# Optimization experiments

Hardware: AMD Instinct MI355X
Metric: run time of the kernel (lower is better)

## Reference

```python
import jax, jax.numpy as jnp
import numpy as np

V, E, H, Ld, NL = 32000, 256, 512, 512, 2   # vocab, embed, enc hidden, latent (=dec hidden), layers
S, T = 1024, 512                            # encoder src len, decoder target len


def setup_inputs() -> dict:
    key = jax.random.key(0)
    ks = jax.random.split(key, 20)
    n = lambda k, shp: jax.random.normal(k, shp, dtype=jnp.float32) * 0.05
    return {
        "x": jax.random.randint(ks[0], (S,), 0, V),
        "y": jax.random.randint(ks[1], (T,), 0, V),
        "emb": n(ks[2], (V, E)),
        # encoder LSTM (input E -> hidden H, 2 layers); bias = b_ih + b_hh combined
        "enc_Wih0": n(ks[3], (4 * H, E)), "enc_Whh0": n(ks[4], (4 * H, H)), "enc_b0": n(ks[5], (4 * H,)),
        "enc_Wih1": n(ks[6], (4 * H, H)), "enc_Whh1": n(ks[7], (4 * H, H)), "enc_b1": n(ks[8], (4 * H,)),
        "enc_fcW": n(ks[9], (Ld, H)), "enc_fcb": n(ks[10], (Ld,)),
        # decoder LSTM: input size is 1 (token id as float!), hidden Ld, 2 layers
        "dec_Wih0": n(ks[11], (4 * Ld, 1)), "dec_Whh0": n(ks[12], (4 * Ld, Ld)), "dec_b0": n(ks[13], (4 * Ld,)),
        "dec_Wih1": n(ks[14], (4 * Ld, Ld)), "dec_Whh1": n(ks[15], (4 * Ld, Ld)), "dec_b1": n(ks[16], (4 * Ld,)),
        "dec_fcW": n(ks[17], (V, Ld)), "dec_fcb": n(ks[18], (V,)),
    }


def _cell(x_in, h, c, Wih, Whh, b):
    # torch LSTM gate order: i, f, g, o
    g = Wih @ x_in + Whh @ h + b
    i, f, gg, o = jnp.split(g, 4)
    c2 = jax.nn.sigmoid(f) * c + jax.nn.sigmoid(i) * jnp.tanh(gg)
    h2 = jax.nn.sigmoid(o) * jnp.tanh(c2)
    return h2, c2


def reference(x, y, emb,
              enc_Wih0, enc_Whh0, enc_b0, enc_Wih1, enc_Whh1, enc_b1,
              enc_fcW, enc_fcb,
              dec_Wih0, dec_Whh0, dec_b0, dec_Wih1, dec_Whh1, dec_b1,
              dec_fcW, dec_fcb):
    encW = [(enc_Wih0, enc_Whh0, enc_b0), (enc_Wih1, enc_Whh1, enc_b1)]
    decW = [(dec_Wih0, dec_Whh0, dec_b0), (dec_Wih1, dec_Whh1, dec_b1)]

    # ---- Encoder: embed + 2-layer LSTM over the source, keep final h ----
    em = emb[x]  # [S, E]

    def enc_step(carry, e_t):
        h, c = carry  # each [NL, H]
        inp = e_t
        hs, cs = [], []
        for l in range(NL):
            Wih, Whh, b = encW[l]
            hl, cl = _cell(inp, h[l], c[l], Wih, Whh, b)
            hs.append(hl); cs.append(cl)
            inp = hl
        return (jnp.stack(hs), jnp.stack(cs)), None

    init = (jnp.zeros((NL, H), jnp.float32), jnp.zeros((NL, H), jnp.float32))
    (h_enc, _), _ = jax.lax.scan(enc_step, init, em)

    z = jax.nn.relu(enc_fcW @ h_enc[-1] + enc_fcb)        # [Ld]
    h0 = jnp.tile(z[None, :], (NL, 1))                    # torch.cat([fc]*num_layers)
    c0 = h0                                               # h_c_enc = h_s_initial in source

    def dec_step(carry, _):
        tok, h, c = carry  # tok: scalar float token id, h/c: [NL, Ld]
        inp = tok[None]    # x.reshape(-1,1).to(float32) with one token -> input dim 1
        hs, cs = [], []
        for l in range(NL):
            Wih, Whh, b = decW[l]
            hl, cl = _cell(inp, h[l], c[l], Wih, Whh, b)
            hs.append(hl); cs.append(cl)
            inp = hl
        logits = dec_fcW @ hs[-1] + dec_fcb               # [V]
        nxt = jnp.argmax(logits).astype(jnp.float32)      # best_guess
        return (nxt, jnp.stack(hs), jnp.stack(cs)), logits

    tok0 = y[0].astype(jnp.float32)
    _, logits_seq = jax.lax.scan(dec_step, (tok0, h0, c0), None, length=T - 1)  # [T-1, V]

    # outputs[0] stays zeros, as in the source (loop starts at i=1); training mode -> raw logits
    return jnp.concatenate([jnp.zeros((1, V), jnp.float32), logits_seq], axis=0)
```

## Files before the change

kernel.cpp:

```cpp
#include <hip/hip_runtime.h>
#include <cmath>

#define NWG 256
#define NTHR 1024

static constexpr int kV = 32000;
static constexpr int kS = 1024;
static constexpr int kT = 512;

static constexpr int kLdsRows = 61;

static constexpr int kOffH0  = kLdsRows * 512;
static constexpr int kOffH1  = kOffH0 + 512;
static constexpr int kOffG   = kOffH1 + 512;
static constexpr int kOffPK  = kOffG + 16;
static constexpr int kOffTok = kOffPK + 32;
static constexpr int kOffB   = kOffTok + 1;
static constexpr int kSmemFloats = kOffB + kLdsRows;
static constexpr unsigned kSmemBytes = ((kSmemFloats * 4 + 255) / 256) * 256;

struct SeqParams {
  const int* x; const int* y;
  const float* emb;
  const float* eWih0; const float* eWhh0; const float* eb0;
  const float* eWih1; const float* eWhh1; const float* eb1;
  const float* efcW;  const float* efcb;
  const float* dWih0; const float* dWhh0; const float* db0;
  const float* dWih1; const float* dWhh1; const float* db1;
  const float* dfcW;  const float* dfcb;
  float* out;
  float* P0;
  unsigned long long* h0e;
  unsigned long long* h1e;
  unsigned long long* h0dB;
  unsigned long long* h1dB;
  unsigned long long* candB;
  unsigned* arrive;
  unsigned* go;
  int decApp;
};

__device__ __forceinline__ float sigmf(float v) { return 1.0f / (1.0f + expf(-v)); }

__device__ __forceinline__ float g_ld(const float* p_) {
  return __hip_atomic_load(p_, __ATOMIC_RELAXED, __HIP_MEMORY_SCOPE_AGENT);
}
__device__ __forceinline__ void g_st(float* p_, float v) {
  __hip_atomic_store(p_, v, __ATOMIC_RELAXED, __HIP_MEMORY_SCOPE_AGENT);
}
__device__ __forceinline__ unsigned long long g_ld64(const unsigned long long* p_) {
  return __hip_atomic_load(p_, __ATOMIC_RELAXED, __HIP_MEMORY_SCOPE_AGENT);
}
__device__ __forceinline__ void g_st64(unsigned long long* p_, unsigned long long v) {
  __hip_atomic_store(p_, v, __ATOMIC_RELAXED, __HIP_MEMORY_SCOPE_AGENT);
}

__device__ __forceinline__ float dot4(float4 a, float4 b) {
  return a.x * b.x + a.y * b.y + a.z * b.z + a.w * b.w;
}
__device__ __forceinline__ float wred(float a) {
  a += __shfl_down(a, 32);
  a += __shfl_down(a, 16);
  a += __shfl_down(a, 8);
  a += __shfl_down(a, 4);
  a += __shfl_down(a, 2);
  a += __shfl_down(a, 1);
  return a;
}
__device__ __forceinline__ int swzg(int g) { return g ^ ((g >> 3) & 7); }

__device__ __forceinline__ void pub_write(unsigned long long* pub, int idx,
                                          unsigned tag, float v) {
  g_st64(&pub[idx],
         ((unsigned long long)tag << 32) | (unsigned long long)__float_as_uint(v));
}

template <int SLP>
__device__ __forceinline__ void poll_stage(const unsigned long long* pub,
                                           unsigned tag, float* dst,
                                           int wave8, int lane) {
  const int idx = (wave8 << 6) | lane;
  unsigned long long x;
  for (;;) {
    x = g_ld64(&pub[idx]);
    if (__all((unsigned)(x >> 32) == tag)) break;
    __builtin_amdgcn_s_sleep(SLP);
  }
  dst[idx] = __uint_as_float((unsigned)x);
}

__device__ __forceinline__ unsigned long long* hrow(unsigned long long* b,
                                                    int app, int s) {
  return b + (size_t)(app ? s : (s & 1)) * 512;
}
__device__ __forceinline__ unsigned long long* crow(unsigned long long* b,
                                                    int app, int t) {
  return b + (app ? (size_t)t * 256 : 0);
}

__device__ void grid_barrier(const SeqParams& p, unsigned gen) {
  __syncthreads();
  const int tid = threadIdx.x;
  if (blockIdx.x == 0) {
    if (tid > 0 && tid < 256) {
      while (__hip_atomic_load(&p.arrive[tid * 32], __ATOMIC_RELAXED,
                               __HIP_MEMORY_SCOPE_AGENT) < gen)
        __builtin_amdgcn_s_sleep(1);
    }
    __syncthreads();
    if (tid > 0 && tid < 256) {
      __hip_atomic_store(&p.go[tid * 32], gen, __ATOMIC_RELAXED,
                         __HIP_MEMORY_SCOPE_AGENT);
    }
  } else {
    if (tid == 0) {
      __hip_atomic_store(&p.arrive[blockIdx.x * 32], gen, __ATOMIC_RELAXED,
                         __HIP_MEMORY_SCOPE_AGENT);
      while (__hip_atomic_load(&p.go[blockIdx.x * 32], __ATOMIC_RELAXED,
                               __HIP_MEMORY_SCOPE_AGENT) < gen)
        __builtin_amdgcn_s_sleep(1);
    }
    __syncthreads();
  }
}

__device__ __forceinline__ unsigned long long pack_cand(float a, int row,
                                                        unsigned tag) {
  const unsigned u = __float_as_uint(a);
  const unsigned key = u ^ (unsigned)(((int)u >> 31) | 0x80000000);
  return ((unsigned long long)key << 32) |
         ((unsigned long long)(0x7FFFu ^ (unsigned)row) << 17) |
         (unsigned long long)tag;
}

__global__ __launch_bounds__(NTHR, 4) void seq2seq_kernel(SeqParams p) {
  extern __shared__ float smem[];
  float* lds_w  = smem;
  float* lds_h0 = smem + kOffH0;
  float* lds_h1 = smem + kOffH1;
  float* lds_g  = smem + kOffG;
  unsigned long long* lds_pk =
      reinterpret_cast<unsigned long long*>(smem + kOffPK);
  float* lds_tok = smem + kOffTok;
  float* lds_b   = smem + kOffB;

  const int w = blockIdx.x;
  const int tid = threadIdx.x;
  const int wave = tid >> 6, lane = tid & 63;
  const int app = p.decApp;

  {
    float* lds_em = lds_w;
    const int t0  = (w & 127) * 8;
    const int row = (w >> 7) * 1024 + tid;
    float4* emv = reinterpret_cast<float4*>(lds_em);
    if (tid < 512) {
      const int tl = tid >> 6, kq = tid & 63;
      const int tk = p.x[t0 + tl];
      emv[tid] = reinterpret_cast<const float4*>(p.emb)[(size_t)tk * 64 + kq];
    }
    __syncthreads();
    float acc[8];
    const float b = p.eb0[row];
#pragma unroll
    for (int t = 0; t < 8; ++t) acc[t] = b;
    for (int kc = 0; kc < 4; ++kc) {
      float4 wv[16];
      const float4* wr =
          reinterpret_cast<const float4*>(p.eWih0 + (size_t)row * 256) + kc * 16;
#pragma unroll
      for (int i = 0; i < 16; ++i) wv[i] = wr[i];
#pragma unroll
      for (int t = 0; t < 8; ++t) {
        const float4* ev =
            reinterpret_cast<const float4*>(lds_em + t * 256) + kc * 16;
        float a = acc[t];
#pragma unroll
        for (int i = 0; i < 16; ++i) a += dot4(wv[i], ev[i]);
        acc[t] = a;
      }
    }
#pragma unroll
    for (int t = 0; t < 8; ++t)
      g_st(&p.P0[(size_t)(t0 + t) * 2048 + row], acc[t]);
    if (tid < 4) {
      if (w < 128) pub_write(p.h0e, w * 4 + tid, 1u, 0.f);
      else         pub_write(p.h1e, (w - 128) * 4 + tid, 1u, 0.f);
    }
    __syncthreads();

    const float4* gw4 =
        reinterpret_cast<const float4*>(p.dfcW + (size_t)w * 125 * 512);
    float4* lw4 = reinterpret_cast<float4*>(lds_w);
    for (int i = tid; i < kLdsRows * 128; i += NTHR)
      lw4[(i & ~127) | ((i & 127) ^ ((i >> 3) & 7))] = gw4[i];
    if (tid < kLdsRows) lds_b[tid] = p.dfcb[w * 125 + tid];
  }
  grid_barrier(p, 1u);

  if (w < 128) {
    const int row_l0 = (wave & 3) * 512 + w * 4 + (wave >> 2);
    float pv_next = 0.f;
    if (lane == 0) pv_next = g_ld(&p.P0[row_l0]);
    float c0e = 0.f;
    for (int i = 0; i < kS; ++i) {
      if (wave < 8)
        poll_stage<2>(p.h0e + (size_t)i * 512, (unsigned)(i + 1), lds_h0,
                      wave, lane);
      __syncthreads();
      const float pv = pv_next;
      if (lane == 0 && i + 1 < kS)
        pv_next = g_ld(&p.P0[(size_t)(i + 1) * 2048 + row_l0]);
      const float4* W4 =
          reinterpret_cast<const float4*>(p.eWhh0 + (size_t)row_l0 * 512);
      const float4* h4 = reinterpret_cast<const float4*>(lds_h0);
      float a = dot4(W4[lane * 2], h4[lane * 2]) +
                dot4(W4[lane * 2 + 1], h4[lane * 2 + 1]);
      a = wred(a);
      if (lane == 0) lds_g[wave] = a + pv;
      __syncthreads();
      if (tid < 4) {
        const float gi = lds_g[tid * 4 + 0];
        const float gf = lds_g[tid * 4 + 1];
        const float gg = lds_g[tid * 4 + 2];
        const float go = lds_g[tid * 4 + 3];
        const float c2 = sigmf(gf) * c0e + sigmf(gi) * tanhf(gg);
        c0e = c2;
        pub_write(p.h0e, (int)((size_t)(i + 1) * 512) + w * 4 + tid,
                  (unsigned)(i + 2), sigmf(go) * tanhf(c2));
      }
    }
  } else {
    const int ww = w - 128;
    const int row = (wave & 3) * 512 + ww * 4 + (wave >> 2);
    float c1e = 0.f;
    for (int j = 0; j < kS; ++j) {
      if (wave < 8)
        poll_stage<2>(p.h0e + (size_t)(j + 1) * 512, (unsigned)(j + 2),
                      lds_h0, wave, lane);
      else
        poll_stage<2>(p.h1e + (size_t)j * 512, (unsigned)(j + 1), lds_h1,
                      wave - 8, lane);
      __syncthreads();
      const float4* Wa =
          reinterpret_cast<const float4*>(p.eWih1 + (size_t)row * 512);
      const float4* Wb =
          reinterpret_cast<const float4*>(p.eWhh1 + (size_t)row * 512);
      const float4* h4a = reinterpret_cast<const float4*>(lds_h0);
      const float4* h4b = reinterpret_cast<const float4*>(lds_h1);
      float a = (lane == 0) ? p.eb1[row] : 0.f;
      a += dot4(Wa[lane * 2], h4a[lane * 2]) +
           dot4(Wa[lane * 2 + 1], h4a[lane * 2 + 1]);
      a += dot4(Wb[lane * 2], h4b[lane * 2]) +
           dot4(Wb[lane * 2 + 1], h4b[lane * 2 + 1]);
      a = wred(a);
      if (lane == 0) lds_g[wave] = a;
      __syncthreads();
      if (tid < 4) {
        const float gi = lds_g[tid * 4 + 0];
        const float gf = lds_g[tid * 4 + 1];
        const float gg = lds_g[tid * 4 + 2];
        const float go = lds_g[tid * 4 + 3];
        const float c2 = sigmf(gf) * c1e + sigmf(gi) * tanhf(gg);
        c1e = c2;
        pub_write(p.h1e, (int)((size_t)(j + 1) * 512) + ww * 4 + tid,
                  (unsigned)(j + 2), sigmf(go) * tanhf(c2));
      }
    }
  }

  float c0d = 0.f, c1d = 0.f;
  {
    if (wave < 8)
      poll_stage<2>(p.h1e + (size_t)kS * 512, (unsigned)(kS + 1), lds_h0,
                    wave, lane);
    __syncthreads();
    if (wave < 2) {
      const int u = w * 2 + wave;
      const float4* W4 =
          reinterpret_cast<const float4*>(p.efcW + (size_t)u * 512);
      const float4* h4 = reinterpret_cast<const float4*>(lds_h0);
      float a = dot4(W4[lane * 2], h4[lane * 2]) +
                dot4(W4[lane * 2 + 1], h4[lane * 2 + 1]);
      a = wred(a);
      if (lane == 0) lds_g[wave] = fmaxf(a + p.efcb[u], 0.f);
    }
    __syncthreads();
    if (tid < 2) {
      const int uu = w * 2 + tid;
      const float z = lds_g[tid];
      c0d = z; c1d = z;
      pub_write(hrow(p.h0dB, app, 0), uu, 1u, z);
      pub_write(hrow(p.h1dB, app, 0), uu, 1u, z);
    }
  }

  float4 Ra0, Rb0, Ra1, Rb1, Ra2, Rb2, Ra3, Rb3;
  float bi0, bi1, bi2, bi3;
  {
    const int rb = w * 125 + kLdsRows + wave * 4;
#define LWR(i)                                                                \
  {                                                                           \
    const float4* q =                                                         \
        reinterpret_cast<const float4*>(p.dfcW + (size_t)(rb + i) * 512) +    \
        lane * 2;                                                             \
    Ra##i = q[0];                                                             \
    Rb##i = q[1];                                                             \
    bi##i = p.dfcb[rb + i];                                                   \
  }
    LWR(0) LWR(1) LWR(2) LWR(3)
#undef LWR
  }
  grid_barrier(p, 2u);

  for (int t = 0; t < kT - 1; ++t) {
    {
      if (wave < 8) {
        poll_stage<2>(hrow(p.h0dB, app, t), (unsigned)(t + 1), lds_h0, wave,
                      lane);
      } else if (wave == 15) {
        if (t == 0) {
          if (lane == 0) lds_tok[0] = (float)p.y[0];
        } else {
          const unsigned tagexp = (unsigned)t;
          const unsigned long long* cb = crow(p.candB, app, t);
          unsigned long long k0, k1, k2, k3;
          for (;;) {
            k0 = g_ld64(&cb[lane]);
            k1 = g_ld64(&cb[lane + 64]);
            k2 = g_ld64(&cb[lane + 128]);
            k3 = g_ld64(&cb[lane + 192]);
            const bool ok = ((unsigned)(k0 & 0x1FFFF) == tagexp) &
                            ((unsigned)(k1 & 0x1FFFF) == tagexp) &
                            ((unsigned)(k2 & 0x1FFFF) == tagexp) &
                            ((unsigned)(k3 & 0x1FFFF) == tagexp);
            if (__all(ok)) break;
            __builtin_amdgcn_s_sleep(1);
          }
          unsigned long long pk = k0;
          if (k1 > pk) pk = k1;
          if (k2 > pk) pk = k2;
          if (k3 > pk) pk = k3;
#pragma unroll
          for (int off = 32; off >= 1; off >>= 1) {
            const unsigned long long o = __shfl_down(pk, off);
            if (o > pk) pk = o;
          }
          if (lane == 0)
            lds_tok[0] = (float)(0x7FFFu ^ (unsigned)((pk >> 17) & 0x7FFF));
        }
      }
      __syncthreads();
      if (wave < 8) {
        const int row = (wave & 3) * 512 + w * 2 + (wave >> 2);
        const float4* W4 =
            reinterpret_cast<const float4*>(p.dWhh0 + (size_t)row * 512);
        const float4* h4 = reinterpret_cast<const float4*>(lds_h0);
        float a = dot4(W4[lane * 2], h4[lane * 2]) +
                  dot4(W4[lane * 2 + 1], h4[lane * 2 + 1]);
        a = wred(a);
        if (lane == 0) lds_g[wave] = a;
      }
      __syncthreads();
      if (tid < 2) {
        const float tok = lds_tok[0];
        const int uu = w * 2 + tid;
        float gv[4];
#pragma unroll
        for (int g = 0; g < 4; ++g) {
          const int rg = g * 512 + uu;
          gv[g] = lds_g[tid * 4 + g] + p.dWih0[rg] * tok + p.db0[rg];
        }
        const float c2 = sigmf(gv[1]) * c0d + sigmf(gv[0]) * tanhf(gv[2]);
        c0d = c2;
        pub_write(hrow(p.h0dB, app, t + 1), uu, (unsigned)(t + 2),
                  sigmf(gv[3]) * tanhf(c2));
      }
    }
    {
      if (wave < 8)
        poll_stage<2>(hrow(p.h0dB, app, t + 1), (unsigned)(t + 2), lds_h0,
                      wave, lane);
      else
        poll_stage<2>(hrow(p.h1dB, app, t), (unsigned)(t + 1), lds_h1,
                      wave - 8, lane);
      __syncthreads();
      if (wave < 8) {
        const int row = (wave & 3) * 512 + w * 2 + (wave >> 2);
        const float4* Wa =
            reinterpret_cast<const float4*>(p.dWih1 + (size_t)row * 512);
        const float4* Wb =
            reinterpret_cast<const float4*>(p.dWhh1 + (size_t)row * 512);
        const float4* h4a = reinterpret_cast<const float4*>(lds_h0);
        const float4* h4b = reinterpret_cast<const float4*>(lds_h1);
        float a = (lane == 0) ? p.db1[row] : 0.f;
        a += dot4(Wa[lane * 2], h4a[lane * 2]) +
             dot4(Wa[lane * 2 + 1], h4a[lane * 2 + 1]);
        a += dot4(Wb[lane * 2], h4b[lane * 2]) +
             dot4(Wb[lane * 2 + 1], h4b[lane * 2 + 1]);
        a = wred(a);
        if (lane == 0) lds_g[wave] = a;
      }
      __syncthreads();
      if (tid < 2) {
        const int uu = w * 2 + tid;
        const float gi = lds_g[tid * 4 + 0];
        const float gf = lds_g[tid * 4 + 1];
        const float gg = lds_g[tid * 4 + 2];
        const float go = lds_g[tid * 4 + 3];
        const float c2 = sigmf(gf) * c1d + sigmf(gi) * tanhf(gg);
        c1d = c2;
        pub_write(hrow(p.h1dB, app, t + 1), uu, (unsigned)(t + 2),
                  sigmf(go) * tanhf(c2));
      }
    }
    {
      if (wave < 8)
        poll_stage<2>(hrow(p.h1dB, app, t + 1), (unsigned)(t + 2), lds_h0,
                      wave, lane);
      __syncthreads();
      const float4* h4 = reinterpret_cast<const float4*>(lds_h0);
      const float4 ha = h4[lane * 2], hb = h4[lane * 2 + 1];
      float* orow = p.out + (size_t)(t + 1) * kV;
      const unsigned tagout = (unsigned)(t + 1);
      unsigned long long best = 0;
      const int rb = w * 125 + kLdsRows + wave * 4;
#define FCR(i)                                                                \
  {                                                                           \
    const int row = rb + i;                                                   \
    float a = (lane == 0) ? bi##i : 0.f;                                      \
    a += dot4(Ra##i, ha) + dot4(Rb##i, hb);                                   \
    a = wred(a);                                                              \
    if (lane == 0) {                                                          \
      orow[row] = a;                                                          \
      const unsigned long long pk2 = pack_cand(a, row, tagout);               \
      if (pk2 > best) best = pk2;                                             \
    }                                                                         \
  }
      FCR(0) FCR(1) FCR(2) FCR(3)
#undef FCR
      const float4* lw4 = reinterpret_cast<const float4*>(lds_w);
      for (int rr = wave; rr < kLdsRows; rr += 16) {
        const int row = w * 125 + rr;
        const float4* lwr = lw4 + rr * 128;
        float a = (lane == 0) ? lds_b[rr] : 0.f;
        a += dot4(lwr[swzg(lane * 2)], ha) + dot4(lwr[swzg(lane * 2 + 1)], hb);
        a = wred(a);
        if (lane == 0) {
          orow[row] = a;
          const unsigned long long pk2 = pack_cand(a, row, tagout);
          if (pk2 > best) best = pk2;
        }
      }
      if (lane == 0) lds_pk[wave] = best;
      __syncthreads();
      if (tid == 0) {
        unsigned long long b2 = lds_pk[0];
#pragma unroll
        for (int k2 = 1; k2 < 16; ++k2)
          if (lds_pk[k2] > b2) b2 = lds_pk[k2];
        g_st64(&crow(p.candB, app, (int)tagout)[w], b2);
      }
    }
  }

  {
    const int idx = w * NTHR + tid;
    if (idx < kV) p.out[idx] = 0.f;
  }
}

extern "C" void kernel_launch(void* const* d_in, const int* in_sizes, int n_in,
                              void* d_out, int out_size, void* d_ws, size_t ws_size,
                              hipStream_t stream) {
  (void)in_sizes; (void)n_in; (void)out_size;
  SeqParams P;
  P.x     = (const int*)d_in[0];
  P.y     = (const int*)d_in[1];
  P.emb   = (const float*)d_in[2];
  P.eWih0 = (const float*)d_in[3];
  P.eWhh0 = (const float*)d_in[4];
  P.eb0   = (const float*)d_in[5];
  P.eWih1 = (const float*)d_in[6];
  P.eWhh1 = (const float*)d_in[7];
  P.eb1   = (const float*)d_in[8];
  P.efcW  = (const float*)d_in[9];
  P.efcb  = (const float*)d_in[10];
  P.dWih0 = (const float*)d_in[11];
  P.dWhh0 = (const float*)d_in[12];
  P.db0   = (const float*)d_in[13];
  P.dWih1 = (const float*)d_in[14];
  P.dWhh1 = (const float*)d_in[15];
  P.db1   = (const float*)d_in[16];
  P.dfcW  = (const float*)d_in[17];
  P.dfcb  = (const float*)d_in[18];
  P.out   = (float*)d_out;

  char* ws = (char*)d_ws;
  P.arrive = (unsigned*)ws;
  P.go     = (unsigned*)(ws + 32768);
  unsigned long long* ringC = (unsigned long long*)(ws + 65536);
  unsigned long long* ring0 = (unsigned long long*)(ws + 67584);
  unsigned long long* ring1 = (unsigned long long*)(ws + 75776);

  const size_t dAppO   = 131072ull;
  const size_t kHdB    = 512ull * 512ull * 8ull;
  const size_t kCdB    = 512ull * 256ull * 8ull;
  const size_t dAppEnd = dAppO + 2 * kHdB + kCdB;
  if (ws_size >= dAppEnd) {
    P.h0dB  = (unsigned long long*)(ws + dAppO);
    P.h1dB  = (unsigned long long*)(ws + dAppO + kHdB);
    P.candB = (unsigned long long*)(ws + dAppO + 2 * kHdB);
    P.decApp = 1;
  } else {
    P.h0dB = ring0; P.h1dB = ring1; P.candB = ringC;
    P.decApp = 0;
  }

  const size_t kP0B = 8388608ull;
  const size_t kEpB = 4198400ull;
  const size_t encO = (dAppEnd + 65535ull) & ~65535ull;
  if (ws_size >= encO + kP0B + 2 * kEpB) {
    P.P0  = (float*)(ws + encO);
    P.h0e = (unsigned long long*)(ws + encO + kP0B);
    P.h1e = (unsigned long long*)(ws + encO + kP0B + kEpB);
  } else {
    char* ob = (char*)d_out;
    P.P0  = (float*)ob;
    P.h0e = (unsigned long long*)(ob + kP0B);
    P.h1e = (unsigned long long*)(ob + kP0B + kEpB);
  }

  (void)hipFuncSetAttribute(reinterpret_cast<const void*>(seq2seq_kernel),
                            hipFuncAttributeMaxDynamicSharedMemorySize,
                            (int)kSmemBytes);

  (void)hipMemsetAsync(d_ws, 0, 83968, stream);

  void* args[] = { &P };
  (void)hipLaunchCooperativeKernel(reinterpret_cast<void*>(seq2seq_kernel),
                                   dim3(NWG), dim3(NTHR), args, kSmemBytes,
                                   stream);
}
```

Measured before the change: 5.602 ms.

## Prefetch published hidden states, swizzle LDS h vectors, use lighter workgroup barriers

Polling of the tagged hidden-state publication buffers now starts with a speculative load issued one stage early, so the first check often succeeds without another global round trip. The argmax candidate buffer is also prefetched ahead of time. Hidden vectors written to LDS are now swizzled to avoid bank conflicts on the float4 reads. __syncthreads is replaced by a barrier that only waits on LDS traffic, not global memory. The aim is to cut latency on the serial recurrent critical path, at the cost of extra global traffic and more complex ordering.

New measurement: 6.123 ms. 9.3% more time.

```diff
diff --git a/kernel.cpp b/kernel.cpp
--- a/kernel.cpp
+++ b/kernel.cpp
@@ -68,6 +68,14 @@
   return a;
 }
 __device__ __forceinline__ int swzg(int g) { return g ^ ((g >> 3) & 7); }
+__device__ __forceinline__ int swzf(int idx) {
+  return (swzg(idx >> 2) << 2) | (idx & 3);
+}
+
+__device__ __forceinline__ void wg_sync() {
+  asm volatile("s_waitcnt lgkmcnt(0)" ::: "memory");
+  __builtin_amdgcn_s_barrier();
+}
 
 __device__ __forceinline__ void pub_write(unsigned long long* pub, int idx,
                                           unsigned tag, float v) {
@@ -76,17 +84,14 @@
 }
 
 template <int SLP>
-__device__ __forceinline__ void poll_stage(const unsigned long long* pub,
-                                           unsigned tag, float* dst,
-                                           int wave8, int lane) {
-  const int idx = (wave8 << 6) | lane;
-  unsigned long long x;
-  for (;;) {
+__device__ __forceinline__ unsigned long long resolve64(
+    unsigned long long x, const unsigned long long* pub, unsigned tag,
+    int idx) {
+  while (!__all((unsigned)(x >> 32) == tag)) {
+    __builtin_amdgcn_s_sleep(SLP);
     x = g_ld64(&pub[idx]);
-    if (__all((unsigned)(x >> 32) == tag)) break;
-    __builtin_amdgcn_s_sleep(SLP);
-  }
-  dst[idx] = __uint_as_float((unsigned)x);
+  }
+  return x;
 }
 
 __device__ __forceinline__ unsigned long long* hrow(unsigned long long* b,
@@ -200,25 +205,31 @@
 
   if (w < 128) {
     const int row_l0 = (wave & 3) * 512 + w * 4 + (wave >> 2);
+    const int idx = (wave << 6) | lane;
     float pv_next = 0.f;
     if (lane == 0) pv_next = g_ld(&p.P0[row_l0]);
+    unsigned long long pf = 0;
+    if (wave < 8) pf = g_ld64(&p.h0e[idx]);
     float c0e = 0.f;
     for (int i = 0; i < kS; ++i) {
-      if (wave < 8)
-        poll_stage<2>(p.h0e + (size_t)i * 512, (unsigned)(i + 1), lds_h0,
-                      wave, lane);
-      __syncthreads();
+      if (wave < 8) {
+        const unsigned long long xx =
+            resolve64<2>(pf, p.h0e + (size_t)i * 512, (unsigned)(i + 1), idx);
+        lds_h0[swzf(idx)] = __uint_as_float((unsigned)xx);
+        pf = g_ld64(&p.h0e[(size_t)(i + 1) * 512 + idx]);
+      }
+      wg_sync();
       const float pv = pv_next;
       if (lane == 0 && i + 1 < kS)
         pv_next = g_ld(&p.P0[(size_t)(i + 1) * 2048 + row_l0]);
       const float4* W4 =
           reinterpret_cast<const float4*>(p.eWhh0 + (size_t)row_l0 * 512);
       const float4* h4 = reinterpret_cast<const float4*>(lds_h0);
-      float a = dot4(W4[lane * 2], h4[lane * 2]) +
-                dot4(W4[lane * 2 + 1], h4[lane * 2 + 1]);
+      float a = dot4(W4[lane * 2], h4[swzg(lane * 2)]) +
+                dot4(W4[lane * 2 + 1], h4[swzg(lane * 2 + 1)]);
       a = wred(a);
       if (lane == 0) lds_g[wave] = a + pv;
-      __syncthreads();
+      wg_sync();
       if (tid < 4) {
         const float gi = lds_g[tid * 4 + 0];
         const float gf = lds_g[tid * 4 + 1];
@@ -233,15 +244,26 @@
   } else {
     const int ww = w - 128;
     const int row = (wave & 3) * 512 + ww * 4 + (wave >> 2);
+    const int idxA = (wave << 6) | lane;
+    const int idxB = ((wave - 8) << 6) | lane;
+    unsigned long long pfA2 = 0, pfB2 = 0;
+    if (wave < 8) pfA2 = g_ld64(&p.h0e[512 + idxA]);
+    else          pfB2 = g_ld64(&p.h1e[idxB]);
     float c1e = 0.f;
     for (int j = 0; j < kS; ++j) {
-      if (wave < 8)
-        poll_stage<2>(p.h0e + (size_t)(j + 1) * 512, (unsigned)(j + 2),
-                      lds_h0, wave, lane);
-      else
-        poll_stage<2>(p.h1e + (size_t)j * 512, (unsigned)(j + 1), lds_h1,
-                      wave - 8, lane);
-      __syncthreads();
+      if (wave < 8) {
+        const unsigned long long xx = resolve64<2>(
+            pfA2, p.h0e + (size_t)(j + 1) * 512, (unsigned)(j + 2), idxA);
+        lds_h0[swzf(idxA)] = __uint_as_float((unsigned)xx);
+        const int nj = (j + 2 <= kS) ? (j + 2) : kS;
+        pfA2 = g_ld64(&p.h0e[(size_t)nj * 512 + idxA]);
+      } else {
+        const unsigned long long xx = resolve64<2>(
+            pfB2, p.h1e + (size_t)j * 512, (unsigned)(j + 1), idxB);
+        lds_h1[swzf(idxB)] = __uint_as_float((unsigned)xx);
+        pfB2 = g_ld64(&p.h1e[(size_t)(j + 1) * 512 + idxB]);
+      }
+      wg_sync();
       const float4* Wa =
           reinterpret_cast<const float4*>(p.eWih1 + (size_t)row * 512);
       const float4* Wb =
@@ -249,13 +271,13 @@
       const float4* h4a = reinterpret_cast<const float4*>(lds_h0);
       const float4* h4b = reinterpret_cast<const float4*>(lds_h1);
       float a = (lane == 0) ? p.eb1[row] : 0.f;
-      a += dot4(Wa[lane * 2], h4a[lane * 2]) +
-           dot4(Wa[lane * 2 + 1], h4a[lane * 2 + 1]);
-      a += dot4(Wb[lane * 2], h4b[lane * 2]) +
-           dot4(Wb[lane * 2 + 1], h4b[lane * 2 + 1]);
+      a += dot4(Wa[lane * 2], h4a[swzg(lane * 2)]) +
+           dot4(Wa[lane * 2 + 1], h4a[swzg(lane * 2 + 1)]);
+      a += dot4(Wb[lane * 2], h4b[swzg(lane * 2)]) +
+           dot4(Wb[lane * 2 + 1], h4b[swzg(lane * 2 + 1)]);
       a = wred(a);
       if (lane == 0) lds_g[wave] = a;
-      __syncthreads();
+      wg_sync();
       if (tid < 4) {
         const float gi = lds_g[tid * 4 + 0];
         const float gf = lds_g[tid * 4 + 1];
@@ -271,17 +293,21 @@
 
   float c0d = 0.f, c1d = 0.f;
   {
-    if (wave < 8)
-      poll_stage<2>(p.h1e + (size_t)kS * 512, (unsigned)(kS + 1), lds_h0,
-                    wave, lane);
+    const int idx = (wave << 6) | lane;
+    if (wave < 8) {
+      const unsigned long long xx =
+          resolve64<2>(g_ld64(&p.h1e[(size_t)kS * 512 + idx]),
+                       p.h1e + (size_t)kS * 512, (unsigned)(kS + 1), idx);
+      lds_h0[swzf(idx)] = __uint_as_float((unsigned)xx);
+    }
     __syncthreads();
     if (wave < 2) {
       const int u = w * 2 + wave;
       const float4* W4 =
           reinterpret_cast<const float4*>(p.efcW + (size_t)u * 512);
       const float4* h4 = reinterpret_cast<const float4*>(lds_h0);
-      float a = dot4(W4[lane * 2], h4[lane * 2]) +
-                dot4(W4[lane * 2 + 1], h4[lane * 2 + 1]);
+      float a = dot4(W4[lane * 2], h4[swzg(lane * 2)]) +
+                dot4(W4[lane * 2 + 1], h4[swzg(lane * 2 + 1)]);
       a = wred(a);
       if (lane == 0) lds_g[wave] = fmaxf(a + p.efcb[u], 0.f);
     }
@@ -311,31 +337,41 @@
     LWR(0) LWR(1) LWR(2) LWR(3)
 #undef LWR
   }
+
+  const int idx  = (wave << 6) | lane;
+  const int idx2 = ((wave - 8) << 6) | lane;
+  unsigned long long pfA = 0, pfD = 0;
+  if (wave < 8) pfA = g_ld64(&hrow(p.h0dB, app, 0)[idx]);
+  else          pfD = g_ld64(&hrow(p.h1dB, app, 0)[idx2]);
+  unsigned long long pk0 = 0, pk1 = 0, pk2 = 0, pk3 = 0;
   grid_barrier(p, 2u);
 
   for (int t = 0; t < kT - 1; ++t) {
+    unsigned long long pfB = 0, pfC = 0, xB = 0;
     {
       if (wave < 8) {
-        poll_stage<2>(hrow(p.h0dB, app, t), (unsigned)(t + 1), lds_h0, wave,
-                      lane);
+        const unsigned long long xx =
+            resolve64<2>(pfA, hrow(p.h0dB, app, t), (unsigned)(t + 1), idx);
+        lds_h0[swzf(idx)] = __uint_as_float((unsigned)xx);
+        pfB = g_ld64(&hrow(p.h0dB, app, t + 1)[idx]);
       } else if (wave == 15) {
         if (t == 0) {
           if (lane == 0) lds_tok[0] = (float)p.y[0];
         } else {
           const unsigned tagexp = (unsigned)t;
           const unsigned long long* cb = crow(p.candB, app, t);
-          unsigned long long k0, k1, k2, k3;
+          unsigned long long k0 = pk0, k1 = pk1, k2 = pk2, k3 = pk3;
           for (;;) {
-            k0 = g_ld64(&cb[lane]);
-            k1 = g_ld64(&cb[lane + 64]);
-            k2 = g_ld64(&cb[lane + 128]);
-            k3 = g_ld64(&cb[lane + 192]);
             const bool ok = ((unsigned)(k0 & 0x1FFFF) == tagexp) &
                             ((unsigned)(k1 & 0x1FFFF) == tagexp) &
                             ((unsigned)(k2 & 0x1FFFF) == tagexp) &
                             ((unsigned)(k3 & 0x1FFFF) == tagexp);
             if (__all(ok)) break;
             __builtin_amdgcn_s_sleep(1);
+            k0 = g_ld64(&cb[lane]);
+            k1 = g_ld64(&cb[lane + 64]);
+            k2 = g_ld64(&cb[lane + 128]);
+            k3 = g_ld64(&cb[lane + 192]);
           }
           unsigned long long pk = k0;
           if (k1 > pk) pk = k1;
@@ -350,18 +386,18 @@
             lds_tok[0] = (float)(0x7FFFu ^ (unsigned)((pk >> 17) & 0x7FFF));
         }
       }
-      __syncthreads();
+      wg_sync();
       if (wave < 8) {
         const int row = (wave & 3) * 512 + w * 2 + (wave >> 2);
         const float4* W4 =
             reinterpret_cast<const float4*>(p.dWhh0 + (size_t)row * 512);
         const float4* h4 = reinterpret_cast<const float4*>(lds_h0);
-        float a = dot4(W4[lane * 2], h4[lane * 2]) +
-                  dot4(W4[lane * 2 + 1], h4[lane * 2 + 1]);
+        float a = dot4(W4[lane * 2], h4[swzg(lane * 2)]) +
+                  dot4(W4[lane * 2 + 1], h4[swzg(lane * 2 + 1)]);
         a = wred(a);
         if (lane == 0) lds_g[wave] = a;
       }
-      __syncthreads();
+      wg_sync();
       if (tid < 2) {
         const float tok = lds_tok[0];
         const int uu = w * 2 + tid;
@@ -378,13 +414,18 @@
       }
     }
     {
-      if (wave < 8)
-        poll_stage<2>(hrow(p.h0dB, app, t + 1), (unsigned)(t + 2), lds_h0,
-                      wave, lane);
-      else
-        poll_stage<2>(hrow(p.h1dB, app, t), (unsigned)(t + 1), lds_h1,
-                      wave - 8, lane);
-      __syncthreads();
+      if (wave < 8) {
+        xB = resolve64<2>(pfB, hrow(p.h0dB, app, t + 1), (unsigned)(t + 2),
+                          idx);
+        lds_h0[swzf(idx)] = __uint_as_float((unsigned)xB);
+        pfC = g_ld64(&hrow(p.h1dB, app, t + 1)[idx]);
+      } else {
+        const unsigned long long xx =
+            resolve64<2>(pfD, hrow(p.h1dB, app, t), (unsigned)(t + 1), idx2);
+        lds_h1[swzf(idx2)] = __uint_as_float((unsigned)xx);
+        pfD = g_ld64(&hrow(p.h1dB, app, t + 1)[idx2]);
+      }
+      wg_sync();
       if (wave < 8) {
         const int row = (wave & 3) * 512 + w * 2 + (wave >> 2);
         const float4* Wa =
@@ -394,14 +435,14 @@
         const float4* h4a = reinterpret_cast<const float4*>(lds_h0);
         const float4* h4b = reinterpret_cast<const float4*>(lds_h1);
         float a = (lane == 0) ? p.db1[row] : 0.f;
-        a += dot4(Wa[lane * 2], h4a[lane * 2]) +
-             dot4(Wa[lane * 2 + 1], h4a[lane * 2 + 1]);
-        a += dot4(Wb[lane * 2], h4b[lane * 2]) +
-             dot4(Wb[lane * 2 + 1], h4b[lane * 2 + 1]);
+        a += dot4(Wa[lane * 2], h4a[swzg(lane * 2)]) +
+             dot4(Wa[lane * 2 + 1], h4a[swzg(lane * 2 + 1)]);
+        a += dot4(Wb[lane * 2], h4b[swzg(lane * 2)]) +
+             dot4(Wb[lane * 2 + 1], h4b[swzg(lane * 2 + 1)]);
         a = wred(a);
         if (lane == 0) lds_g[wave] = a;
       }
-      __syncthreads();
+      wg_sync();
       if (tid < 2) {
         const int uu = w * 2 + tid;
         const float gi = lds_g[tid * 4 + 0];
@@ -415,12 +456,15 @@
       }
     }
     {
-      if (wave < 8)
-        poll_stage<2>(hrow(p.h1dB, app, t + 1), (unsigned)(t + 2), lds_h0,
-                      wave, lane);
-      __syncthreads();
+      if (wave < 8) {
+        const unsigned long long xC = resolve64<2>(
+            pfC, hrow(p.h1dB, app, t + 1), (unsigned)(t + 2), idx);
+        lds_h0[swzf(idx)] = __uint_as_float((unsigned)xC);
+        pfA = xB;
+      }
+      wg_sync();
       const float4* h4 = reinterpret_cast<const float4*>(lds_h0);
-      const float4 ha = h4[lane * 2], hb = h4[lane * 2 + 1];
+      const float4 ha = h4[swzg(lane * 2)], hb = h4[swzg(lane * 2 + 1)];
       float* orow = p.out + (size_t)(t + 1) * kV;
       const unsigned tagout = (unsigned)(t + 1);
       unsigned long long best = 0;
@@ -433,8 +477,8 @@
     a = wred(a);                                                              \
     if (lane == 0) {                                                          \
       orow[row] = a;                                                          \
-      const unsigned long long pk2 = pack_cand(a, row, tagout);               \
-      if (pk2 > best) best = pk2;                                             \
+      const unsigned long long pk2_ = pack_cand(a, row, tagout);              \
+      if (pk2_ > best) best = pk2_;                                           \
     }                                                                         \
   }
       FCR(0) FCR(1) FCR(2) FCR(3)
@@ -448,12 +492,12 @@
         a = wred(a);
         if (lane == 0) {
           orow[row] = a;
-          const unsigned long long pk2 = pack_cand(a, row, tagout);
-          if (pk2 > best) best = pk2;
+          const unsigned long long pk2_ = pack_cand(a, row, tagout);
+          if (pk2_ > best) best = pk2_;
         }
       }
       if (lane == 0) lds_pk[wave] = best;
-      __syncthreads();
+      wg_sync();
       if (tid == 0) {
         unsigned long long b2 = lds_pk[0];
 #pragma unroll
@@ -461,12 +505,19 @@
           if (lds_pk[k2] > b2) b2 = lds_pk[k2];
         g_st64(&crow(p.candB, app, (int)tagout)[w], b2);
       }
+      if (wave == 15) {
+        const unsigned long long* cb2 = crow(p.candB, app, t + 1);
+        pk0 = g_ld64(&cb2[lane]);
+        pk1 = g_ld64(&cb2[lane + 64]);
+        pk2 = g_ld64(&cb2[lane + 128]);
+        pk3 = g_ld64(&cb2[lane + 192]);
+      }
     }
   }
 
   {
-    const int idx = w * NTHR + tid;
-    if (idx < kV) p.out[idx] = 0.f;
+    const int oidx = w * NTHR + tid;
+    if (oidx < kV) p.out[oidx] = 0.f;
   }
 }
 
```
